# Optimization experiments

Hardware: AMD Instinct MI355X
Metric: run time of the kernel (lower is better)

The kernel has to match this reference:

```python
import jax, jax.numpy as jnp
import numpy as np

N_HEADS = 16  # must match init_kwargs
BIAS_SCALE = 0.1


def _src_grid(out_size, in_size):
    # torch F.interpolate bilinear, align_corners=False semantics
    scale = in_size / out_size
    src = jnp.clip((jnp.arange(out_size, dtype=jnp.float32) + 0.5) * scale - 0.5, 0.0)
    i0 = jnp.minimum(jnp.floor(src).astype(jnp.int32), in_size - 1)
    i1 = jnp.minimum(i0 + 1, in_size - 1)
    w = src - i0.astype(jnp.float32)
    return i0, i1, w


def _bilinear_resize(img, out_h, out_w):
    Hin, Win = img.shape[-2], img.shape[-1]
    r0, r1, wy = _src_grid(out_h, Hin)
    c0, c1, wx = _src_grid(out_w, Win)
    rows = img[:, r0, :] * (1.0 - wy)[None, :, None] + img[:, r1, :] * wy[None, :, None]
    return rows[:, :, c0] * (1.0 - wx)[None, None, :] + rows[:, :, c1] * wx[None, None, :]


def setup_inputs() -> dict:
    key = jax.random.key(0)
    ks = jax.random.split(key, 10)
    B, L, D, M, K = 4, 1024, 1024, 64, 32
    s = 0.02
    return {
        "x": jax.random.normal(ks[0], (B, L, D), dtype=jnp.float32),
        "harmonics": jax.random.normal(ks[1], (B, M, K), dtype=jnp.float32),
        "wq": jax.random.normal(ks[2], (D, D), dtype=jnp.float32) * s,
        "bq": jax.random.normal(ks[3], (D,), dtype=jnp.float32) * s,
        "wk": jax.random.normal(ks[4], (D, D), dtype=jnp.float32) * s,
        "bk": jax.random.normal(ks[5], (D,), dtype=jnp.float32) * s,
        "wv": jax.random.normal(ks[6], (D, D), dtype=jnp.float32) * s,
        "bv": jax.random.normal(ks[7], (D,), dtype=jnp.float32) * s,
        "wo": jax.random.normal(ks[8], (D, D), dtype=jnp.float32) * s,
        "bo": jax.random.normal(ks[9], (D,), dtype=jnp.float32) * s,
    }


def reference(x, harmonics, wq, bq, wk, bk, wv, bv, wo, bo):
    B, L, D = x.shape
    hd = D // N_HEADS
    scaling = hd ** -0.5

    def split_heads(t):  # [B, L, D] -> [B, H, L, hd]
        return t.reshape(B, L, N_HEADS, hd).transpose(0, 2, 1, 3)

    q = split_heads(x @ wq.T + bq)
    k = split_heads(x @ wk.T + bk)
    v = split_heads(x @ wv.T + bv)

    scores = jnp.einsum("bhqd,bhkd->bhqk", q, k) * scaling  # [B, H, L, L]

    gram = jnp.einsum("bmk,bnk->bmn", harmonics, harmonics)  # [B, M, M]
    bias = _bilinear_resize(gram, L, L)  # [B, L, L]
    scores = scores + BIAS_SCALE * bias[:, None, :, :]

    attn = jax.nn.softmax(scores, axis=-1)
    out = jnp.einsum("bhqk,bhkd->bhqd", attn, v)  # [B, H, L, hd]
    out = out.transpose(0, 2, 1, 3).reshape(B, L, D)
    return out @ wo.T + bo
```

## Files before the change

kernel.cpp:

```cpp
#include <hip/hip_runtime.h>


using short8  = __attribute__((ext_vector_type(8))) short;
using short4v = __attribute__((ext_vector_type(4))) short;
using float4v = __attribute__((ext_vector_type(4))) float;

#define MFMA16(a, b, c) __builtin_amdgcn_mfma_f32_16x16x32_bf16((a), (b), (c), 0, 0, 0)

#define LOG2E 1.44269504088896f

static __device__ __forceinline__ short f2bf(float f) {
    union { float f; unsigned u; } v; v.f = f;
    unsigned r = v.u + 0x7fffu + ((v.u >> 16) & 1u);
    return (short)(r >> 16);
}

static __device__ __forceinline__ unsigned pack2bf(float lo, float hi) {
    union { float f; unsigned u; } a, b;
    a.f = lo; b.f = hi;
    return __builtin_amdgcn_perm(b.u + 0x8000u, a.u + 0x8000u, 0x07060302u);
}

static __device__ __forceinline__ void dma16(const short* g, short* l) {
    __builtin_amdgcn_global_load_lds((const __attribute__((address_space(1))) void*)g,
                                     (__attribute__((address_space(3))) void*)l, 16, 0, 0);
}

__global__ __launch_bounds__(256) void convert_all(
    const float* __restrict__ x,  const float* __restrict__ wq,
    const float* __restrict__ wk, const float* __restrict__ wv,
    const float* __restrict__ wo, short* __restrict__ xb, short* __restrict__ wb) {
    int idx = blockIdx.x * 256 + threadIdx.x;
    for (int i = idx; i < 2097152; i += gridDim.x * 256) {
        const float* src; short* dst;
        if (i < 1048576) {
            src = x + (size_t)i * 4;
            dst = xb + (size_t)i * 4;
        } else {
            int j = i - 1048576;
            int sel = j >> 18;
            const float* w = (sel == 0) ? wq : (sel == 1) ? wk : (sel == 2) ? wv : wo;
            src = w + (size_t)(j & 262143) * 4;
            dst = wb + (size_t)j * 4;
        }
        float4v v = *(const float4v*)src;
        short4v o;
        o.x = f2bf(v.x); o.y = f2bf(v.y); o.z = f2bf(v.z); o.w = f2bf(v.w);
        *(short4v*)dst = o;
    }
}

__global__ __launch_bounds__(256) void fill_aug(const float* __restrict__ harm,
                                                short* __restrict__ Qp,
                                                short* __restrict__ Kp) {
    int b  = blockIdx.y;
    int lc = blockIdx.x;
    int tid = threadIdx.x;
    int ll = tid >> 3;
    int d8 = (tid & 7) * 8;
    int l  = lc * 32 + ll;

    __shared__ float hs[64][33];
    for (int i = tid; i < 2048; i += 256) hs[i >> 5][i & 31] = harm[(size_t)b * 2048 + i];
    __syncthreads();

    float src = (l + 0.5f) * 0.0625f - 0.5f;
    if (src < 0.f) src = 0.f;
    int r0 = (int)floorf(src); if (r0 > 63) r0 = 63;
    int r1 = r0 + 1;           if (r1 > 63) r1 = 63;
    float wy = src - (float)r0;

    float hr[32];
    #pragma unroll
    for (int k = 0; k < 32; k++) hr[k] = (1.f - wy) * hs[r0][k] + wy * hs[r1][k];

    short8 qa, ka;
    #pragma unroll
    for (int j = 0; j < 8; j++) {
        float g = 0.f;
        #pragma unroll
        for (int k = 0; k < 32; k++) g += hr[k] * hs[d8 + j][k];
        qa[j] = f2bf(0.1f * LOG2E * g);
    }
    #pragma unroll
    for (int j = 0; j < 8; j++) {
        float vv = 0.f;
        if (d8 + j == r0) vv += 1.f - wy;
        if (d8 + j == r1) vv += wy;
        ka[j] = f2bf(vv);
    }
    for (int h = 0; h < 16; h++) {
        size_t base = (((size_t)(b * 16 + h) * 1024 + l) << 7) + 64 + d8;
        *(short8*)(Qp + base) = qa;
        *(short8*)(Kp + base) = ka;
    }
}

template <int MODE>
__global__ __launch_bounds__(256, 2) void gemm_kernel(
    const short* __restrict__ A,
    const short* __restrict__ Wb,
    const float* __restrict__ B0, const float* __restrict__ B1, const float* __restrict__ B2,
    short* __restrict__ Qp, short* __restrict__ Kp, short* __restrict__ Vp,
    float* __restrict__ outF) {
    const int z = blockIdx.z;
    const short* W  = Wb + (size_t)z * 1048576;
    const float* Bs = (z == 0) ? B0 : ((z == 1) ? B1 : B2);

    __shared__ short Sm[2][8192];

    const int tid  = threadIdx.x;
    const int lane = tid & 63;
    const int wv   = tid >> 6;
    const int wm   = (wv >> 1) * 64;
    const int wn   = (wv & 1) * 64;
    const int l16  = lane & 15;
    const int quad = lane >> 4;
    const int bm   = blockIdx.x * 128;
    const int bn   = blockIdx.y * 128;

    const short* aSrc[2];
    const short* wSrc[2];
    #pragma unroll
    for (int j = 0; j < 2; j++) {
        int c = j * 256 + tid;
        int r = c >> 2, gs = (c & 3) ^ ((r >> 1) & 3);
        aSrc[j] = A + (size_t)(bm + r) * 1024 + gs * 8;
        wSrc[j] = W + (size_t)(bn + r) * 1024 + gs * 8;
    }
    const int fr = (quad ^ ((l16 >> 1) & 3)) * 8;
    int ai[4], bi[4];
    #pragma unroll
    for (int t = 0; t < 4; t++) {
        ai[t] = (wm + t * 16 + l16) * 32 + fr;
        bi[t] = 4096 + (wn + t * 16 + l16) * 32 + fr;
    }

    float4v zero4 = {0.f, 0.f, 0.f, 0.f};
    float4v acc[4][4];
    #pragma unroll
    for (int i = 0; i < 4; i++)
        #pragma unroll
        for (int j = 0; j < 4; j++) acc[i][j] = zero4;

    dma16(aSrc[0], &Sm[0][wv * 512]);
    dma16(aSrc[1], &Sm[0][2048 + wv * 512]);
    dma16(wSrc[0], &Sm[0][4096 + wv * 512]);
    dma16(wSrc[1], &Sm[0][6144 + wv * 512]);
    #pragma unroll
    for (int j = 0; j < 2; j++) { aSrc[j] += 32; wSrc[j] += 32; }
    __syncthreads();

    for (int kt = 0; kt < 32; kt++) {
        const int cur = kt & 1, nxt = cur ^ 1;
        if (kt < 31) {
            dma16(aSrc[0], &Sm[nxt][wv * 512]);
            dma16(aSrc[1], &Sm[nxt][2048 + wv * 512]);
            dma16(wSrc[0], &Sm[nxt][4096 + wv * 512]);
            dma16(wSrc[1], &Sm[nxt][6144 + wv * 512]);
            #pragma unroll
            for (int j = 0; j < 2; j++) { aSrc[j] += 32; wSrc[j] += 32; }
        }

        short8 af[4], bfr[4];
        #pragma unroll
        for (int mt = 0; mt < 4; mt++) af[mt]  = *(const short8*)&Sm[cur][ai[mt]];
        #pragma unroll
        for (int nt = 0; nt < 4; nt++) bfr[nt] = *(const short8*)&Sm[cur][bi[nt]];
        #pragma unroll
        for (int mt = 0; mt < 4; mt++)
            #pragma unroll
            for (int nt = 0; nt < 4; nt++)
                acc[mt][nt] = MFMA16(af[mt], bfr[nt], acc[mt][nt]);

        __syncthreads();
    }

    #pragma unroll
    for (int mt = 0; mt < 4; mt++)
        #pragma unroll
        for (int nt = 0; nt < 4; nt++) {
            int col = bn + wn + nt * 16 + l16;
            float bias = Bs[col];
            #pragma unroll
            for (int r = 0; r < 4; r++) {
                int row = bm + wm + mt * 16 + quad * 4 + r;
                float val = acc[mt][nt][r] + bias;
                if (MODE == 1) {
                    outF[(size_t)row * 1024 + col] = val;
                } else {
                    int b = row >> 10, l = row & 1023;
                    int h = col >> 6,  d = col & 63;
                    size_t bhl = (size_t)(b * 16 + h) * 1024 + l;
                    if (z == 0)      Qp[(bhl << 7) + d] = f2bf(val * (0.125f * LOG2E));
                    else if (z == 1) Kp[(bhl << 7) + d] = f2bf(val);
                    else {
                        int slot = (l & ~31) | (((l >> 2) & 3) << 3) |
                                   (((l >> 4) & 1) << 2) | (l & 3);
                        Vp[(((size_t)(b * 16 + h) * 64 + d) << 10) + slot] = f2bf(val);
                    }
                }
            }
        }
}

__global__ __launch_bounds__(256, 2)
void flash_kernel(const short* __restrict__ Qp,
                  const short* __restrict__ Kp,
                  const short* __restrict__ Vp,
                  short* __restrict__ AO) {
    const int h  = blockIdx.x;
    const int qb = blockIdx.y;
    const int b  = blockIdx.z;
    const int tid  = threadIdx.x;
    const int lane = tid & 63;
    const int w    = tid >> 6;
    const int l16  = lane & 15;
    const int quad = lane >> 4;
    const size_t bh = (size_t)(b * 16 + h);

    __shared__ short Ks[16384];
    __shared__ short Vs[8192];

    short8 qf[2][4];
    #pragma unroll
    for (int u = 0; u < 2; u++) {
        const short* Qb = Qp + ((bh * 1024 + qb * 128 + w * 32 + u * 16 + l16) << 7) + quad * 8;
        #pragma unroll
        for (int c = 0; c < 4; c++) qf[u][c] = *(const short8*)(Qb + c * 32);
    }

    const short* kSrc[4];
    #pragma unroll
    for (int jj = 0; jj < 4; jj++) {
        int key = w * 16 + jj * 4 + quad;
        kSrc[jj] = Kp + (bh << 17) + key * 128 + ((l16 ^ (key & 15)) * 8);
    }
    const short* vSrc[2];
    #pragma unroll
    for (int g = 0; g < 2; g++) {
        int d = w * 16 + g * 8 + (lane >> 3);
        vSrc[g] = Vp + (bh << 16) + d * 1024 + (((lane & 7) ^ (d & 7)) * 8);
    }

    int krd[4];
    #pragma unroll
    for (int c = 0; c < 4; c++) krd[c] = l16 * 128 + (((c * 4 + quad) ^ l16) * 8);
    int vrd[2];
    #pragma unroll
    for (int g = 0; g < 2; g++) vrd[g] = l16 * 64 + (((g * 4 + quad) ^ (l16 & 7)) * 8);

    #pragma unroll
    for (int jj = 0; jj < 4; jj++) dma16(kSrc[jj], &Ks[w * 2048 + jj * 512]);
    #pragma unroll
    for (int g = 0; g < 2; g++) dma16(vSrc[g], &Vs[w * 1024 + g * 512]);
    #pragma unroll
    for (int jj = 0; jj < 4; jj++) kSrc[jj] += 8192;
    #pragma unroll
    for (int g = 0; g < 2; g++) vSrc[g] += 64;
    int dstK = 8192, dstV = 4096;

    float4v zero4 = {0.f, 0.f, 0.f, 0.f};
    float4v o_acc[2][4];
    #pragma unroll
    for (int u = 0; u < 2; u++)
        #pragma unroll
        for (int mt = 0; mt < 4; mt++) o_acc[u][mt] = zero4;
    float l_part[2] = {0.f, 0.f};

    __syncthreads();

    for (int kt = 0; kt < 16; kt++) {
        if (kt < 15) {
            #pragma unroll
            for (int jj = 0; jj < 4; jj++) dma16(kSrc[jj], &Ks[dstK + w * 2048 + jj * 512]);
            #pragma unroll
            for (int g = 0; g < 2; g++) dma16(vSrc[g], &Vs[dstV + w * 1024 + g * 512]);
            #pragma unroll
            for (int jj = 0; jj < 4; jj++) kSrc[jj] += 8192;
            #pragma unroll
            for (int g = 0; g < 2; g++) vSrc[g] += 64;
            dstK ^= 8192; dstV ^= 4096;
        }

        float4v s[2][4];
        #pragma unroll
        for (int mt = 0; mt < 4; mt++) {
            short8 kf[4];
            #pragma unroll
            for (int c = 0; c < 4; c++) kf[c] = *(const short8*)&Ks[krd[c] + mt * 2048];
            #pragma unroll
            for (int u = 0; u < 2; u++) {
                s[u][mt] = MFMA16(kf[0], qf[u][0], zero4);
                #pragma unroll
                for (int c = 1; c < 4; c++)
                    s[u][mt] = MFMA16(kf[c], qf[u][c], s[u][mt]);
            }
        }

        #pragma unroll
        for (int u = 0; u < 2; u++)
            #pragma unroll
            for (int mt = 0; mt < 4; mt++)
                #pragma unroll
                for (int r = 0; r < 4; r++) {
                    float p = __builtin_exp2f(s[u][mt][r]);
                    s[u][mt][r] = p;
                    l_part[u] += p;
                }

        #pragma unroll
        for (int g = 0; g < 2; g++) {
            short8 pf[2];
            #pragma unroll
            for (int u = 0; u < 2; u++) {
                union { unsigned uu[4]; short8 v; } t;
                t.uu[0] = pack2bf(s[u][2 * g][0], s[u][2 * g][1]);
                t.uu[1] = pack2bf(s[u][2 * g][2], s[u][2 * g][3]);
                t.uu[2] = pack2bf(s[u][2 * g + 1][0], s[u][2 * g + 1][1]);
                t.uu[3] = pack2bf(s[u][2 * g + 1][2], s[u][2 * g + 1][3]);
                pf[u] = t.v;
            }
            #pragma unroll
            for (int mt = 0; mt < 4; mt++) {
                short8 vf = *(const short8*)&Vs[vrd[g] + mt * 1024];
                #pragma unroll
                for (int u = 0; u < 2; u++)
                    o_acc[u][mt] = MFMA16(vf, pf[u], o_acc[u][mt]);
            }
        }

        if (kt < 15) __syncthreads();
        #pragma unroll
        for (int c = 0; c < 4; c++) krd[c] ^= 8192;
        #pragma unroll
        for (int g = 0; g < 2; g++) vrd[g] ^= 4096;
    }

    #pragma unroll
    for (int u = 0; u < 2; u++) {
        float l = l_part[u];
        l += __shfl_xor(l, 16, 64);
        l += __shfl_xor(l, 32, 64);
        float inv = 1.0f / l;
        int row = b * 1024 + qb * 128 + w * 32 + u * 16 + l16;
        #pragma unroll
        for (int mt = 0; mt < 4; mt++) {
            short4v ov;
            #pragma unroll
            for (int r = 0; r < 4; r++) ov[r] = f2bf(o_acc[u][mt][r] * inv);
            *(short4v*)(AO + (size_t)row * 1024 + h * 64 + mt * 16 + quad * 4) = ov;
        }
    }
}

extern "C" void kernel_launch(void* const* d_in, const int* in_sizes, int n_in,
                              void* d_out, int out_size, void* d_ws, size_t ws_size,
                              hipStream_t stream) {
    const float* x    = (const float*)d_in[0];
    const float* harm = (const float*)d_in[1];
    const float* wq   = (const float*)d_in[2];
    const float* bq   = (const float*)d_in[3];
    const float* wk   = (const float*)d_in[4];
    const float* bk   = (const float*)d_in[5];
    const float* wv   = (const float*)d_in[6];
    const float* bv   = (const float*)d_in[7];
    const float* wo   = (const float*)d_in[8];
    const float* bo   = (const float*)d_in[9];
    float* outF = (float*)d_out;

    short* xb   = (short*)d_ws;
    short* Qp   = xb + (size_t)4 * 1048576;
    short* Kp   = Qp + (size_t)8 * 1048576;
    short* Vp   = Kp + (size_t)8 * 1048576;
    short* Wqkv = Vp + (size_t)4 * 1048576;
    short* Wob  = Wqkv + (size_t)3 * 1048576;
    short* AO   = xb;

    convert_all<<<dim3(2048), dim3(256), 0, stream>>>(x, wq, wk, wv, wo, xb, Wqkv);
    gemm_kernel<0><<<dim3(32, 8, 3), dim3(256), 0, stream>>>(
        xb, Wqkv, bq, bk, bv, Qp, Kp, Vp, nullptr);
    fill_aug<<<dim3(32, 4), dim3(256), 0, stream>>>(harm, Qp, Kp);
    flash_kernel<<<dim3(16, 8, 4), dim3(256), 0, stream>>>(Qp, Kp, Vp, AO);
    gemm_kernel<1><<<dim3(32, 8, 1), dim3(256), 0, stream>>>(
        AO, Wob, bo, nullptr, nullptr, nullptr, nullptr, nullptr, outF);
}
```

Before: 192.9 us.

## Triple-buffer K/V tiles in flash kernel with partial vmcnt waits

Grows the K/V shared-memory staging from two buffers to three and prefetches two tiles ahead. __syncthreads is replaced with a partial s_waitcnt vmcnt plus a raw barrier, so the newest tile's loads can stay in flight across iterations. The row-sum accumulation is also split into four independent lanes to shorten the serial add chain. More LDS per block (72KB) may cut occupancy under launch_bounds(256,2), and the hand-counted vmcnt values must match the DMA count exactly.

After: 193.2 us. No clear change (+0.2%).

```diff
diff --git a/kernel.cpp b/kernel.cpp
--- a/kernel.cpp
+++ b/kernel.cpp
@@ -219,8 +219,8 @@
     const int quad = lane >> 4;
     const size_t bh = (size_t)(b * 16 + h);
 
-    __shared__ short Ks[16384];
-    __shared__ short Vs[8192];
+    __shared__ short Ks[24576];
+    __shared__ short Vs[12288];
 
     short8 qf[2][4];
     #pragma unroll
@@ -258,7 +258,14 @@
     for (int jj = 0; jj < 4; jj++) kSrc[jj] += 8192;
     #pragma unroll
     for (int g = 0; g < 2; g++) vSrc[g] += 64;
-    int dstK = 8192, dstV = 4096;
+    #pragma unroll
+    for (int jj = 0; jj < 4; jj++) dma16(kSrc[jj], &Ks[8192 + w * 2048 + jj * 512]);
+    #pragma unroll
+    for (int g = 0; g < 2; g++) dma16(vSrc[g], &Vs[4096 + w * 1024 + g * 512]);
+    #pragma unroll
+    for (int jj = 0; jj < 4; jj++) kSrc[jj] += 8192;
+    #pragma unroll
+    for (int g = 0; g < 2; g++) vSrc[g] += 64;
 
     float4v zero4 = {0.f, 0.f, 0.f, 0.f};
     float4v o_acc[2][4];
@@ -266,29 +273,37 @@
     for (int u = 0; u < 2; u++)
         #pragma unroll
         for (int mt = 0; mt < 4; mt++) o_acc[u][mt] = zero4;
-    float l_part[2] = {0.f, 0.f};
-
-    __syncthreads();
+    float4v l_acc[2] = {zero4, zero4};
+
+    asm volatile("s_waitcnt vmcnt(6)" ::: "memory");
+    __builtin_amdgcn_s_barrier();
+    __builtin_amdgcn_sched_barrier(0);
+
+    int bufR = 0;
+    int bufW = 2;
 
     for (int kt = 0; kt < 16; kt++) {
-        if (kt < 15) {
-            #pragma unroll
-            for (int jj = 0; jj < 4; jj++) dma16(kSrc[jj], &Ks[dstK + w * 2048 + jj * 512]);
-            #pragma unroll
-            for (int g = 0; g < 2; g++) dma16(vSrc[g], &Vs[dstV + w * 1024 + g * 512]);
+        if (kt < 14) {
+            const int wb = bufW << 13;
+            const int wv2 = bufW << 12;
+            #pragma unroll
+            for (int jj = 0; jj < 4; jj++) dma16(kSrc[jj], &Ks[wb + w * 2048 + jj * 512]);
+            #pragma unroll
+            for (int g = 0; g < 2; g++) dma16(vSrc[g], &Vs[wv2 + w * 1024 + g * 512]);
             #pragma unroll
             for (int jj = 0; jj < 4; jj++) kSrc[jj] += 8192;
             #pragma unroll
             for (int g = 0; g < 2; g++) vSrc[g] += 64;
-            dstK ^= 8192; dstV ^= 4096;
-        }
+        }
+        const int kb = bufR << 13;
+        const int vb = bufR << 12;
 
         float4v s[2][4];
         #pragma unroll
         for (int mt = 0; mt < 4; mt++) {
             short8 kf[4];
             #pragma unroll
-            for (int c = 0; c < 4; c++) kf[c] = *(const short8*)&Ks[krd[c] + mt * 2048];
+            for (int c = 0; c < 4; c++) kf[c] = *(const short8*)&Ks[kb + krd[c] + mt * 2048];
             #pragma unroll
             for (int u = 0; u < 2; u++) {
                 s[u][mt] = MFMA16(kf[0], qf[u][0], zero4);
@@ -301,13 +316,14 @@
         #pragma unroll
         for (int u = 0; u < 2; u++)
             #pragma unroll
-            for (int mt = 0; mt < 4; mt++)
+            for (int mt = 0; mt < 4; mt++) {
                 #pragma unroll
-                for (int r = 0; r < 4; r++) {
-                    float p = __builtin_exp2f(s[u][mt][r]);
-                    s[u][mt][r] = p;
-                    l_part[u] += p;
-                }
+                for (int r = 0; r < 4; r++)
+                    s[u][mt][r] = __builtin_exp2f(s[u][mt][r]);
+                #pragma unroll
+                for (int r = 0; r < 4; r++)
+                    l_acc[u][r] += s[u][mt][r];
+            }
 
         #pragma unroll
         for (int g = 0; g < 2; g++) {
@@ -323,23 +339,29 @@
             }
             #pragma unroll
             for (int mt = 0; mt < 4; mt++) {
-                short8 vf = *(const short8*)&Vs[vrd[g] + mt * 1024];
+                short8 vf = *(const short8*)&Vs[vb + vrd[g] + mt * 1024];
                 #pragma unroll
                 for (int u = 0; u < 2; u++)
                     o_acc[u][mt] = MFMA16(vf, pf[u], o_acc[u][mt]);
             }
         }
 
-        if (kt < 15) __syncthreads();
-        #pragma unroll
-        for (int c = 0; c < 4; c++) krd[c] ^= 8192;
-        #pragma unroll
-        for (int g = 0; g < 2; g++) vrd[g] ^= 4096;
+        if (kt < 15) {
+            if (kt < 14) {
+                asm volatile("s_waitcnt vmcnt(6)" ::: "memory");
+            } else {
+                asm volatile("s_waitcnt vmcnt(0)" ::: "memory");
+            }
+            __builtin_amdgcn_s_barrier();
+            __builtin_amdgcn_sched_barrier(0);
+        }
+        bufR = (bufR >= 2) ? 0 : bufR + 1;
+        bufW = (bufW >= 2) ? 0 : bufW + 1;
     }
 
     #pragma unroll
     for (int u = 0; u < 2; u++) {
-        float l = l_part[u];
+        float l = l_acc[u][0] + l_acc[u][1] + l_acc[u][2] + l_acc[u][3];
         l += __shfl_xor(l, 16, 64);
         l += __shfl_xor(l, 32, 64);
         float inv = 1.0f / l;
```
